# Kernel tuning notes

Measured on AMD Instinct MI355X. Metric: run time of the kernel, lower is better.

## Reference

```python
import jax, jax.numpy as jnp
import numpy as np

TOKENS, INPUT_DIM, NUM_EXPERTS, TOP_K = 16384, 2048, 64, 2


def setup_inputs() -> dict:
    key = jax.random.key(0)
    k1, k2 = jax.random.split(key)
    x = jax.random.normal(k1, (TOKENS, INPUT_DIM), dtype=jnp.float32)
    # nn.Linear weight is [out, in]; scale like torch default init
    W = jax.random.normal(k2, (NUM_EXPERTS, INPUT_DIM), dtype=jnp.float32) * (1.0 / np.sqrt(INPUT_DIM))
    b = jnp.zeros((NUM_EXPERTS,), dtype=jnp.float32)
    return {"x": x, "W": W, "b": b}


def reference(x, W, b):
    # logits = x @ W.T + b  -> [tokens, num_experts]
    logits = jnp.einsum("td,ed->te", x, W) + b
    top_k_vals, top_k_indices = jax.lax.top_k(logits, TOP_K)
    router_probs = jax.nn.softmax(top_k_vals, axis=1)
    return router_probs, top_k_indices, logits
```

## Files before the change

kernel.cpp:

```cpp
#include <hip/hip_runtime.h>
#include <math.h>

#define TOKENS 16384
#define DIM    2048
#define NE     64
#define BT     32
#define KC     32
#define SLICE_K (DIM / 2)
#define NPHASE (SLICE_K / KC)

__global__ __launch_bounds__(256) void wtrans_kernel(const float* __restrict__ W,
                                                     float* __restrict__ wt) {
    const int k0 = blockIdx.x * 8;
    const int ts = threadIdx.x;
    const int e  = ts & 63;
    const int jr = ts >> 6;
    float2 v = *(const float2*)&W[(size_t)e * DIM + k0 + jr * 2];
    wt[(size_t)(k0 + jr * 2    ) * NE + e] = v.x;
    wt[(size_t)(k0 + jr * 2 + 1) * NE + e] = v.y;
}

__device__ __forceinline__ void async_f4(const float* g, float* l) {
    __builtin_amdgcn_global_load_lds((const __attribute__((address_space(1))) void*)g,
                                     (__attribute__((address_space(3))) void*)l,
                                     16, 0, 0);
}

__global__ __launch_bounds__(512, 4) void router_kernel(const float* __restrict__ x,
                                                        const float* __restrict__ wt,
                                                        const float* __restrict__ b,
                                                        float* __restrict__ out) {
    __shared__ __align__(16) float lds[12288];

    const int tid  = threadIdx.x;
    const int s    = tid >> 8;
    const int ts   = tid & 255;
    const int wv   = ts >> 6;
    const int lane = tid & 63;
    const int t0   = blockIdx.x * BT;

    const int xrow = ts >> 3, xcol = ts & 7;
    const float* gxp = x + (size_t)(t0 + xrow) * DIM + s * SLICE_K
                         + ((xcol ^ (xrow & 7)) * 4);
    const float* gwp = wt + (size_t)s * SLICE_K * NE + ts * 4;

    float* lx[2]; float* lw0[2]; float* lw1[2];
    #pragma unroll
    for (int bb = 0; bb < 2; ++bb) {
        float* base = &lds[s * 3072 + bb * 6144];
        lx[bb]  = base + (wv * 64) * 4;
        lw0[bb] = base + 1024 + (wv * 64) * 4;
        lw1[bb] = base + 1024 + (256 + wv * 64) * 4;
    }

    auto stage = [&](int kc, int bb) {
        const float* gw = gwp + (size_t)kc * KC * NE;
        async_f4(gxp + kc * KC, lx[bb]);
        async_f4(gw,            lw0[bb]);
        async_f4(gw + 1024,     lw1[bb]);
    };

    const int eg = ts & 15;
    const int tg = ts >> 4;

    float acc[2][4] = {};

    stage(0, 0);
    __syncthreads();

    for (int kc = 0; kc < NPHASE; ++kc) {
        const int cur = kc & 1;
        if (kc + 1 < NPHASE) stage(kc + 1, cur ^ 1);

        const float* base = &lds[s * 3072 + cur * 6144];
        const float4* x4 = (const float4*)base;
        const float4* w4 = (const float4*)(base + 1024);

        #pragma unroll 2
        for (int c = 0; c < 8; ++c) {
            float4 xa[2], wa[4];
            #pragma unroll
            for (int i = 0; i < 2; ++i) {
                const int r = tg * 2 + i;
                xa[i] = x4[r * 8 + (c ^ (r & 7))];
            }
            #pragma unroll
            for (int j = 0; j < 4; ++j) wa[j] = w4[(c * 4 + j) * 16 + eg];
            #pragma unroll
            for (int i = 0; i < 2; ++i) {
                const float* xi = (const float*)&xa[i];
                #pragma unroll
                for (int kx = 0; kx < 4; ++kx) {
                    const float* wj = (const float*)&wa[kx];
                    acc[i][0] += xi[kx] * wj[0];
                    acc[i][1] += xi[kx] * wj[1];
                    acc[i][2] += xi[kx] * wj[2];
                    acc[i][3] += xi[kx] * wj[3];
                }
            }
        }
        __syncthreads();
    }

    float4* red = (float4*)&lds[0];
    if (s == 1) {
        #pragma unroll
        for (int i = 0; i < 2; ++i)
            red[i * 256 + ts] = make_float4(acc[i][0], acc[i][1], acc[i][2], acc[i][3]);
    }
    __syncthreads();

    float* logt = &lds[2048];
    if (s == 0) {
        const float4 bb4 = *(const float4*)&b[eg * 4];
        float* logits_out = out + (size_t)TOKENS * 4;
        #pragma unroll
        for (int i = 0; i < 2; ++i) {
            float4 r = red[i * 256 + ts];
            float4 v;
            v.x = acc[i][0] + r.x + bb4.x;
            v.y = acc[i][1] + r.y + bb4.y;
            v.z = acc[i][2] + r.z + bb4.z;
            v.w = acc[i][3] + r.w + bb4.w;
            const int t = tg * 2 + i;
            *(float4*)&logits_out[(size_t)(t0 + t) * NE + eg * 4] = v;
            *(float4*)&logt[t * NE + eg * 4] = v;
        }
    }
    __syncthreads();

    const int wvg = tid >> 6;
    for (int r = 0; r < 4; ++r) {
        const int t = wvg * 4 + r;
        const float v = logt[t * NE + lane];

        float v1 = v; int i1 = lane;
        #pragma unroll
        for (int off = 32; off >= 1; off >>= 1) {
            float ov = __shfl_xor(v1, off, 64);
            int   oi = __shfl_xor(i1, off, 64);
            if (ov > v1 || (ov == v1 && oi < i1)) { v1 = ov; i1 = oi; }
        }
        float vm = (lane == i1) ? -INFINITY : v;
        float v2 = vm; int i2 = lane;
        #pragma unroll
        for (int off = 32; off >= 1; off >>= 1) {
            float ov = __shfl_xor(v2, off, 64);
            int   oi = __shfl_xor(i2, off, 64);
            if (ov > v2 || (ov == v2 && oi < i2)) { v2 = ov; i2 = oi; }
        }

        if (lane == 0) {
            const int tok = t0 + t;
            float e1 = expf(v2 - v1);
            float sden = 1.0f + e1;
            out[(size_t)tok * 2 + 0] = 1.0f / sden;
            out[(size_t)tok * 2 + 1] = e1 / sden;
            float* idxf = out + (size_t)TOKENS * 2;
            idxf[(size_t)tok * 2 + 0] = (float)i1;
            idxf[(size_t)tok * 2 + 1] = (float)i2;
        }
    }
}

extern "C" void kernel_launch(void* const* d_in, const int* in_sizes, int n_in,
                              void* d_out, int out_size, void* d_ws, size_t ws_size,
                              hipStream_t stream) {
    const float* x = (const float*)d_in[0];
    const float* W = (const float*)d_in[1];
    const float* b = (const float*)d_in[2];
    float* out = (float*)d_out;
    float* wt = (float*)d_ws;

    wtrans_kernel<<<DIM / 8, 256, 0, stream>>>(W, wt);
    router_kernel<<<TOKENS / BT, 512, 0, stream>>>(x, wt, b, out);
}
```

Baseline: 236.9 us.

## Drop W transpose kernel; read x via wave-uniform loads and stage W in padded LDS

Removes the separate weight-transpose launch and stages W row-major into a padded LDS tile through register double buffering. Each wave now owns eight tokens and one K-half. Each lane holds one expert's weights in registers, and x is read straight from global memory with wave-uniform (broadcast) loads instead of going through LDS. The top-k and softmax are fused into the same waves that do the final reduction. This cuts one launch and the x LDS traffic, but relies on the cache for x reuse and replaces async LDS loads with synchronous register staging.

```diff
diff --git a/kernel.cpp b/kernel.cpp
--- a/kernel.cpp
+++ b/kernel.cpp
@@ -5,160 +5,133 @@
 #define DIM    2048
 #define NE     64
 #define BT     32
+#define TW     8
 #define KC     32
-#define SLICE_K (DIM / 2)
-#define NPHASE (SLICE_K / KC)
-
-__global__ __launch_bounds__(256) void wtrans_kernel(const float* __restrict__ W,
-                                                     float* __restrict__ wt) {
-    const int k0 = blockIdx.x * 8;
-    const int ts = threadIdx.x;
-    const int e  = ts & 63;
-    const int jr = ts >> 6;
-    float2 v = *(const float2*)&W[(size_t)e * DIM + k0 + jr * 2];
-    wt[(size_t)(k0 + jr * 2    ) * NE + e] = v.x;
-    wt[(size_t)(k0 + jr * 2 + 1) * NE + e] = v.y;
-}
-
-__device__ __forceinline__ void async_f4(const float* g, float* l) {
-    __builtin_amdgcn_global_load_lds((const __attribute__((address_space(1))) void*)g,
-                                     (__attribute__((address_space(3))) void*)l,
-                                     16, 0, 0);
-}
+#define HALFK  (DIM / 2)
+#define NPH    (HALFK / KC)
+#define WSTR   36
+#define WTILE  (NE * WSTR)
 
 __global__ __launch_bounds__(512, 4) void router_kernel(const float* __restrict__ x,
-                                                        const float* __restrict__ wt,
+                                                        const float* __restrict__ W,
                                                         const float* __restrict__ b,
                                                         float* __restrict__ out) {
-    __shared__ __align__(16) float lds[12288];
+    __shared__ __align__(16) float lds[2 * 2 * WTILE];
 
-    const int tid  = threadIdx.x;
-    const int s    = tid >> 8;
-    const int ts   = tid & 255;
-    const int wv   = ts >> 6;
+    const int tid = threadIdx.x;
+
+    const int sh  = tid >> 8;
+    const int ts  = tid & 255;
+    const int e_s = ts >> 2;
+    const int kq  = (ts & 3) * 8;
+
+    const int wid  = __builtin_amdgcn_readfirstlane(tid >> 6);
+    const int h    = wid & 1;
+    const int tg   = wid >> 1;
     const int lane = tid & 63;
     const int t0   = blockIdx.x * BT;
 
-    const int xrow = ts >> 3, xcol = ts & 7;
-    const float* gxp = x + (size_t)(t0 + xrow) * DIM + s * SLICE_K
-                         + ((xcol ^ (xrow & 7)) * 4);
-    const float* gwp = wt + (size_t)s * SLICE_K * NE + ts * 4;
+    const float* __restrict__ gw = W + (size_t)e_s * DIM + sh * HALFK + kq;
+    const float* __restrict__ xbase = x + (size_t)(t0 + tg * TW) * DIM + h * HALFK;
 
-    float* lx[2]; float* lw0[2]; float* lw1[2];
+    float4 acc[TW];
     #pragma unroll
-    for (int bb = 0; bb < 2; ++bb) {
-        float* base = &lds[s * 3072 + bb * 6144];
-        lx[bb]  = base + (wv * 64) * 4;
-        lw0[bb] = base + 1024 + (wv * 64) * 4;
-        lw1[bb] = base + 1024 + (256 + wv * 64) * 4;
+    for (int t = 0; t < TW; ++t) acc[t] = make_float4(0.f, 0.f, 0.f, 0.f);
+
+    {
+        float4 g0 = *(const float4*)(gw);
+        float4 g1 = *(const float4*)(gw + 4);
+        float* d = &lds[(0 * 2 + sh) * WTILE + e_s * WSTR + kq];
+        *(float4*)(d)     = g0;
+        *(float4*)(d + 4) = g1;
     }
-
-    auto stage = [&](int kc, int bb) {
-        const float* gw = gwp + (size_t)kc * KC * NE;
-        async_f4(gxp + kc * KC, lx[bb]);
-        async_f4(gw,            lw0[bb]);
-        async_f4(gw + 1024,     lw1[bb]);
-    };
-
-    const int eg = ts & 15;
-    const int tg = ts >> 4;
-
-    float acc[2][4] = {};
-
-    stage(0, 0);
     __syncthreads();
 
-    for (int kc = 0; kc < NPHASE; ++kc) {
+    for (int kc = 0; kc < NPH; ++kc) {
         const int cur = kc & 1;
-        if (kc + 1 < NPHASE) stage(kc + 1, cur ^ 1);
 
-        const float* base = &lds[s * 3072 + cur * 6144];
-        const float4* x4 = (const float4*)base;
-        const float4* w4 = (const float4*)(base + 1024);
+        float4 g0, g1;
+        if (kc + 1 < NPH) {
+            const float* gsrc = gw + (kc + 1) * KC;
+            g0 = *(const float4*)(gsrc);
+            g1 = *(const float4*)(gsrc + 4);
+        }
 
-        #pragma unroll 2
-        for (int c = 0; c < 8; ++c) {
-            float4 xa[2], wa[4];
+        float4 wreg[8];
+        {
+            const float* wr = &lds[(cur * 2 + h) * WTILE + lane * WSTR];
             #pragma unroll
-            for (int i = 0; i < 2; ++i) {
-                const int r = tg * 2 + i;
-                xa[i] = x4[r * 8 + (c ^ (r & 7))];
+            for (int j = 0; j < 8; ++j) wreg[j] = *(const float4*)(wr + 4 * j);
+        }
+
+        #pragma unroll
+        for (int t = 0; t < TW; ++t) {
+            const float4* __restrict__ xp =
+                (const float4*)(xbase + (size_t)t * DIM + kc * KC);
+            float4 a = acc[t];
+            #pragma unroll
+            for (int j = 0; j < 8; ++j) {
+                const float4 xv = xp[j];
+                a.x += xv.x * wreg[j].x;
+                a.y += xv.y * wreg[j].y;
+                a.z += xv.z * wreg[j].z;
+                a.w += xv.w * wreg[j].w;
             }
-            #pragma unroll
-            for (int j = 0; j < 4; ++j) wa[j] = w4[(c * 4 + j) * 16 + eg];
-            #pragma unroll
-            for (int i = 0; i < 2; ++i) {
-                const float* xi = (const float*)&xa[i];
-                #pragma unroll
-                for (int kx = 0; kx < 4; ++kx) {
-                    const float* wj = (const float*)&wa[kx];
-                    acc[i][0] += xi[kx] * wj[0];
-                    acc[i][1] += xi[kx] * wj[1];
-                    acc[i][2] += xi[kx] * wj[2];
-                    acc[i][3] += xi[kx] * wj[3];
-                }
-            }
+            acc[t] = a;
+        }
+
+        if (kc + 1 < NPH) {
+            float* d = &lds[((cur ^ 1) * 2 + sh) * WTILE + e_s * WSTR + kq];
+            *(float4*)(d)     = g0;
+            *(float4*)(d + 4) = g1;
         }
         __syncthreads();
     }
 
-    float4* red = (float4*)&lds[0];
-    if (s == 1) {
+    float lg[TW];
+    #pragma unroll
+    for (int t = 0; t < TW; ++t)
+        lg[t] = (acc[t].x + acc[t].y) + (acc[t].z + acc[t].w);
+
+    if (h == 1) {
         #pragma unroll
-        for (int i = 0; i < 2; ++i)
-            red[i * 256 + ts] = make_float4(acc[i][0], acc[i][1], acc[i][2], acc[i][3]);
+        for (int t = 0; t < TW; ++t)
+            lds[tg * (TW * NE) + t * NE + lane] = lg[t];
     }
     __syncthreads();
 
-    float* logt = &lds[2048];
-    if (s == 0) {
-        const float4 bb4 = *(const float4*)&b[eg * 4];
+    if (h == 0) {
+        const float bv = b[lane];
         float* logits_out = out + (size_t)TOKENS * 4;
+        float* idxf = out + (size_t)TOKENS * 2;
         #pragma unroll
-        for (int i = 0; i < 2; ++i) {
-            float4 r = red[i * 256 + ts];
-            float4 v;
-            v.x = acc[i][0] + r.x + bb4.x;
-            v.y = acc[i][1] + r.y + bb4.y;
-            v.z = acc[i][2] + r.z + bb4.z;
-            v.w = acc[i][3] + r.w + bb4.w;
-            const int t = tg * 2 + i;
-            *(float4*)&logits_out[(size_t)(t0 + t) * NE + eg * 4] = v;
-            *(float4*)&logt[t * NE + eg * 4] = v;
-        }
-    }
-    __syncthreads();
+        for (int t = 0; t < TW; ++t) {
+            const float v = lg[t] + lds[tg * (TW * NE) + t * NE + lane] + bv;
+            const int tok = t0 + tg * TW + t;
+            logits_out[(size_t)tok * NE + lane] = v;
 
-    const int wvg = tid >> 6;
-    for (int r = 0; r < 4; ++r) {
-        const int t = wvg * 4 + r;
-        const float v = logt[t * NE + lane];
+            float v1 = v; int i1 = lane;
+            #pragma unroll
+            for (int off = 32; off >= 1; off >>= 1) {
+                float ov = __shfl_xor(v1, off, 64);
+                int   oi = __shfl_xor(i1, off, 64);
+                if (ov > v1 || (ov == v1 && oi < i1)) { v1 = ov; i1 = oi; }
+            }
+            float vm = (lane == i1) ? -INFINITY : v;
+            float v2 = vm; int i2 = lane;
+            #pragma unroll
+            for (int off = 32; off >= 1; off >>= 1) {
+                float ov = __shfl_xor(v2, off, 64);
+                int   oi = __shfl_xor(i2, off, 64);
+                if (ov > v2 || (ov == v2 && oi < i2)) { v2 = ov; i2 = oi; }
+            }
 
-        float v1 = v; int i1 = lane;
-        #pragma unroll
-        for (int off = 32; off >= 1; off >>= 1) {
-            float ov = __shfl_xor(v1, off, 64);
-            int   oi = __shfl_xor(i1, off, 64);
-            if (ov > v1 || (ov == v1 && oi < i1)) { v1 = ov; i1 = oi; }
-        }
-        float vm = (lane == i1) ? -INFINITY : v;
-        float v2 = vm; int i2 = lane;
-        #pragma unroll
-        for (int off = 32; off >= 1; off >>= 1) {
-            float ov = __shfl_xor(v2, off, 64);
-            int   oi = __shfl_xor(i2, off, 64);
-            if (ov > v2 || (ov == v2 && oi < i2)) { v2 = ov; i2 = oi; }
-        }
-
-        if (lane == 0) {
-            const int tok = t0 + t;
-            float e1 = expf(v2 - v1);
-            float sden = 1.0f + e1;
-            out[(size_t)tok * 2 + 0] = 1.0f / sden;
-            out[(size_t)tok * 2 + 1] = e1 / sden;
-            float* idxf = out + (size_t)TOKENS * 2;
-            idxf[(size_t)tok * 2 + 0] = (float)i1;
-            idxf[(size_t)tok * 2 + 1] = (float)i2;
+            if (lane == 0) {
+                float e1 = expf(v2 - v1);
+                float sden = 1.0f + e1;
+                *(float2*)&out[(size_t)tok * 2] = make_float2(1.0f / sden, e1 / sden);
+                *(float2*)&idxf[(size_t)tok * 2] = make_float2((float)i1, (float)i2);
+            }
         }
     }
 }
@@ -170,8 +143,6 @@
     const float* W = (const float*)d_in[1];
     const float* b = (const float*)d_in[2];
     float* out = (float*)d_out;
-    float* wt = (float*)d_ws;
 
-    wtrans_kernel<<<DIM / 8, 256, 0, stream>>>(W, wt);
-    router_kernel<<<TOKENS / BT, 512, 0, stream>>>(x, wt, b, out);
+    router_kernel<<<TOKENS / BT, 512, 0, stream>>>(x, W, b, out);
 }
```

New measurement: 311.5 us. 31.5% more time.
